# Optimization experiments

Hardware: AMD Instinct MI355X
Metric: run time of the kernel (lower is better)

Reference implementation:

```python
import jax, jax.numpy as jnp
import numpy as np

LOG_2PI = float(np.log(2.0 * np.pi))


def setup_inputs() -> dict:
    key = jax.random.key(0)
    k1, k2, k3 = jax.random.split(key, 3)
    N, D, K = 2_000_000, 16, 32
    data = jax.random.normal(k1, (N, D), dtype=jnp.float32)
    means = jax.random.uniform(k2, (K, D), dtype=jnp.float32)  # torch.rand init
    # torch init is eye expanded per component; perturb slightly so the
    # Cholesky / solve paths are exercised with non-trivial values while
    # A @ A.T stays well-conditioned PD.
    cov_parts = (jnp.eye(D, dtype=jnp.float32)[None, :, :]
                 + 0.1 * jax.random.normal(k3, (K, D, D), dtype=jnp.float32))
    log_weights = jnp.zeros((K,), dtype=jnp.float32)
    return {"data": data, "means": means, "cov_parts": cov_parts,
            "log_weights": log_weights}


def _mixture_loglik(data, means, cov_parts, log_weights):
    D = data.shape[-1]
    # covariance_k = A_k @ A_k^T  -> Cholesky factor L_k (lower)
    cov = jnp.einsum('kij,klj->kil', cov_parts, cov_parts)      # [K, D, D]
    chol = jnp.linalg.cholesky(cov)                             # [K, D, D]

    def comp_logprob(mu, L):
        # MVN log_prob for one component over all N points
        diff = data - mu                                        # [N, D]
        # solve L z = diff^T  -> z: [D, N]
        z = jax.scipy.linalg.solve_triangular(L, diff.T, lower=True)
        quad = jnp.sum(z * z, axis=0)                           # [N]
        logdet = jnp.sum(jnp.log(jnp.diagonal(L)))              # 0.5*logdet(cov)
        return -0.5 * (quad + D * LOG_2PI) - logdet             # [N]

    # [N, K] log-likelihood per point per component
    log_liks = jax.vmap(comp_logprob, in_axes=(0, 0), out_axes=1)(means, chol)
    weighted = log_liks + log_weights ** 2                      # note: squared, per source
    return jnp.mean(jax.nn.logsumexp(weighted, axis=1))


def reference(data, means, cov_parts, log_weights):
    return _mixture_loglik(data, means, cov_parts, log_weights)
```

## Files before the change

### kernel.cpp

```cpp
#include <hip/hip_runtime.h>
#include <math.h>


#define LOG_2PI 1.8378770664093453f
#define INV_LN2 1.4426950408889634f
#define LN2_D   0.6931471805599453

typedef float    float4v __attribute__((ext_vector_type(4)));
typedef float    f32x16  __attribute__((ext_vector_type(16)));
typedef _Float16 f16x8   __attribute__((ext_vector_type(8)));
typedef _Float16 f16x2   __attribute__((ext_vector_type(2)));

union H8 { f16x8 h8; f16x2 h2[4]; };

#if __has_builtin(__builtin_amdgcn_exp2f)
#define EXP2F(x) __builtin_amdgcn_exp2f(x)
#else
#define EXP2F(x) exp2f(x)
#endif
#if __has_builtin(__builtin_amdgcn_logf)
#define LOG2F(x) __builtin_amdgcn_logf(x)
#else
#define LOG2F(x) log2f(x)
#endif

static __device__ __forceinline__ f16x2 pk2(float a, float b) {
#if __has_builtin(__builtin_amdgcn_cvt_pkrtz)
  return __builtin_bit_cast(f16x2, __builtin_amdgcn_cvt_pkrtz(a, b));
#else
  f16x2 r; r[0] = (_Float16)a; r[1] = (_Float16)b; return r;
#endif
}

static __device__ __forceinline__ float partner32(float x, bool lo) {
#if __has_builtin(__builtin_amdgcn_permlane32_swap)
  typedef unsigned u32x2 __attribute__((ext_vector_type(2)));
  unsigned u = __builtin_bit_cast(unsigned, x);
  u32x2 r = __builtin_amdgcn_permlane32_swap(u, u, false, false);
  return __builtin_bit_cast(float, lo ? r[1] : r[0]);
#else
  return __shfl_xor(x, 32, 64);
#endif
}

static __device__ __forceinline__ f16x2 sel2(bool c, f16x2 a, f16x2 b) {
  unsigned ua = __builtin_bit_cast(unsigned, a);
  unsigned ub = __builtin_bit_cast(unsigned, b);
  return __builtin_bit_cast(f16x2, c ? ua : ub);
}

__global__ void setup_kernel(const float* __restrict__ means,
                             const float* __restrict__ cov_parts,
                             const float* __restrict__ log_weights,
                             _Float16* __restrict__ W)
{
  const int k = blockIdx.x;
  const int i = threadIdx.x;

  __shared__ float sA[16][17];
  __shared__ float sC[16][17];
  __shared__ float sMu[16];
  __shared__ float sR[16];

  if (i < 16) {
    #pragma unroll
    for (int j = 0; j < 16; ++j) sA[i][j] = cov_parts[(k*16 + i)*16 + j];
    sMu[i] = means[k*16 + i];
  }
  __syncthreads();

  if (i < 16) {
    #pragma unroll
    for (int j = 0; j < 16; ++j) {
      float acc = 0.f;
      #pragma unroll
      for (int l = 0; l < 16; ++l) acc += sA[i][l] * sA[j][l];
      sC[i][j] = acc;
    }
  }
  __syncthreads();

  for (int j = 0; j < 16; ++j) {
    if (i == j) {
      float d = sC[j][j];
      for (int l = 0; l < j; ++l) d -= sC[j][l]*sC[j][l];
      sC[j][j] = sqrtf(d);
    }
    __syncthreads();
    if (i < 16 && i > j) {
      float a = sC[i][j];
      for (int l = 0; l < j; ++l) a -= sC[i][l]*sC[j][l];
      sC[i][j] = a / sC[j][j];
    }
    __syncthreads();
  }

  if (i < 16) {
    float y[16];
    #pragma unroll
    for (int r = 0; r < 16; ++r) {
      float a = (r == i) ? 1.f : 0.f;
      #pragma unroll
      for (int l = 0; l < r; ++l) a -= sC[r][l] * y[l];
      y[r] = a / sC[r][r];
    }
    #pragma unroll
    for (int r = 0; r < 16; ++r) sA[r][i] = y[r];
  }
  __syncthreads();

  if (i < 16) {
    float p[16];
    #pragma unroll
    for (int j = 0; j < 16; ++j) {
      float acc = 0.f;
      #pragma unroll
      for (int l = 0; l < 16; ++l) acc += sA[l][i] * sA[l][j];
      p[j] = acc;
    }
    float ri = 0.f;
    #pragma unroll
    for (int j = 0; j < 16; ++j) ri += p[j] * sMu[j];
    sR[i] = ri;

    #pragma unroll
    for (int j = 0; j < 16; ++j) {
      W[(size_t)(i*64 + (k + 32*(j >> 3)))*8 + (j & 7)] =
          (_Float16)(-0.5f * INV_LN2 * p[j]);
    }
    W[(size_t)(16*64 + (k + 32*(i >> 3)))*8 + (i & 7)] =
        (_Float16)(INV_LN2 * ri);
  }
  __syncthreads();

  if (i == 0) {
    float logdet = 0.f;
    #pragma unroll
    for (int j = 0; j < 16; ++j) logdet += __logf(sC[j][j]);
    float mupmu = 0.f;
    #pragma unroll
    for (int j = 0; j < 16; ++j) mupmu += sMu[j] * sR[j];
    float lw = log_weights[k];
    float c2v = INV_LN2 * (-0.5f*(mupmu + 16.f*LOG_2PI) - logdet + lw*lw);
    #pragma unroll
    for (int v = 0; v < 8; ++v) {
      W[(size_t)(17*64 + k)*8 + v]      = (v == 0) ? (_Float16)c2v : (_Float16)0.f;
      W[(size_t)(17*64 + k + 32)*8 + v] = (_Float16)0.f;
    }
  }
}

__global__ __launch_bounds__(256, 2) void main_kernel(
    const float* __restrict__ data,
    const _Float16* __restrict__ W,
    float* __restrict__ partials,
    int npairs)
{
  const int lane = threadIdx.x & 63;
  const int n32  = lane & 31;
  const bool lo  = lane < 32;
  const int gwave  = (int)((blockIdx.x * blockDim.x + threadIdx.x) >> 6);
  const int nwaves = (int)((gridDim.x * blockDim.x) >> 6);

  f16x8 Wf[18];
  #pragma unroll
  for (int c = 0; c < 18; ++c)
    Wf[c] = *(const f16x8*)(W + (size_t)(c*64 + lane)*8);

  H8 bC;
  #pragma unroll
  for (int j = 0; j < 4; ++j) bC.h2[j] = pk2(0.f, 0.f);
  if (lo) bC.h2[0] = pk2(1.f, 0.f);

  float accsum = 0.f;

  const char* ptr = (const char*)data + ((size_t)gwave*4096 + (size_t)n32*64);
  const size_t step = (size_t)nwaves * 4096;

  float4v pA0, pA1, pA2, pA3, pB0, pB1, pB2, pB3;
  if (gwave < npairs) {
    pA0 = *(const float4v*)(ptr);        pA1 = *(const float4v*)(ptr + 16);
    pA2 = *(const float4v*)(ptr + 32);   pA3 = *(const float4v*)(ptr + 48);
    pB0 = *(const float4v*)(ptr + 2048); pB1 = *(const float4v*)(ptr + 2064);
    pB2 = *(const float4v*)(ptr + 2080); pB3 = *(const float4v*)(ptr + 2096);
  }

  for (int p = gwave; p < npairs; p += nwaves) {
    f16x2 xhA[8], xhB[8];
    xhA[0] = pk2(pA0[0], pA0[1]); xhA[1] = pk2(pA0[2], pA0[3]);
    xhA[2] = pk2(pA1[0], pA1[1]); xhA[3] = pk2(pA1[2], pA1[3]);
    xhA[4] = pk2(pA2[0], pA2[1]); xhA[5] = pk2(pA2[2], pA2[3]);
    xhA[6] = pk2(pA3[0], pA3[1]); xhA[7] = pk2(pA3[2], pA3[3]);
    xhB[0] = pk2(pB0[0], pB0[1]); xhB[1] = pk2(pB0[2], pB0[3]);
    xhB[2] = pk2(pB1[0], pB1[1]); xhB[3] = pk2(pB1[2], pB1[3]);
    xhB[4] = pk2(pB2[0], pB2[1]); xhB[5] = pk2(pB2[2], pB2[3]);
    xhB[6] = pk2(pB3[0], pB3[1]); xhB[7] = pk2(pB3[2], pB3[3]);

    ptr += step;
    if (p + nwaves < npairs) {
      pA0 = *(const float4v*)(ptr);        pA1 = *(const float4v*)(ptr + 16);
      pA2 = *(const float4v*)(ptr + 32);   pA3 = *(const float4v*)(ptr + 48);
      pB0 = *(const float4v*)(ptr + 2048); pB1 = *(const float4v*)(ptr + 2064);
      pB2 = *(const float4v*)(ptr + 2080); pB3 = *(const float4v*)(ptr + 2096);
    }

    f16x2 xsA[4], xsB[4];
    #pragma unroll
    for (int j = 0; j < 4; ++j) {
      xsA[j] = sel2(lo, xhA[j], xhA[4+j]);
      xsB[j] = sel2(lo, xhB[j], xhB[4+j]);
    }

    f32x16 accA, accB;
    #pragma unroll
    for (int r = 0; r < 16; ++r) { accA[r] = 0.f; accB[r] = 0.f; }

    #pragma unroll
    for (int c = 0; c < 16; ++c) {
      _Float16 xiA = xhA[c >> 1][c & 1];
      H8 bA;
      #pragma unroll
      for (int j = 0; j < 4; ++j) bA.h2[j] = xsA[j] * xiA;
      accA = __builtin_amdgcn_mfma_f32_32x32x16_f16(Wf[c], bA.h8, accA, 0, 0, 0);
      _Float16 xiB = xhB[c >> 1][c & 1];
      H8 bB;
      #pragma unroll
      for (int j = 0; j < 4; ++j) bB.h2[j] = xsB[j] * xiB;
      accB = __builtin_amdgcn_mfma_f32_32x32x16_f16(Wf[c], bB.h8, accB, 0, 0, 0);
    }
    {
      H8 bA, bB;
      #pragma unroll
      for (int j = 0; j < 4; ++j) { bA.h2[j] = xsA[j]; bB.h2[j] = xsB[j]; }
      accA = __builtin_amdgcn_mfma_f32_32x32x16_f16(Wf[16], bA.h8, accA, 0, 0, 0);
      accB = __builtin_amdgcn_mfma_f32_32x32x16_f16(Wf[16], bB.h8, accB, 0, 0, 0);
    }
    {
      accA = __builtin_amdgcn_mfma_f32_32x32x16_f16(Wf[17], bC.h8, accA, 0, 0, 0);
      accB = __builtin_amdgcn_mfma_f32_32x32x16_f16(Wf[17], bC.h8, accB, 0, 0, 0);
    }

    {
      float m = accA[0];
      #pragma unroll
      for (int r = 1; r < 16; ++r) m = fmaxf(m, accA[r]);
      m = fmaxf(m, partner32(m, lo));
      float s = 0.f;
      #pragma unroll
      for (int r = 0; r < 16; ++r) s += EXP2F(accA[r] - m);
      s += partner32(s, lo);
      accsum += m + LOG2F(s);
    }
    {
      float m = accB[0];
      #pragma unroll
      for (int r = 1; r < 16; ++r) m = fmaxf(m, accB[r]);
      m = fmaxf(m, partner32(m, lo));
      float s = 0.f;
      #pragma unroll
      for (int r = 0; r < 16; ++r) s += EXP2F(accB[r] - m);
      s += partner32(s, lo);
      accsum += m + LOG2F(s);
    }
  }

  #pragma unroll
  for (int off = 1; off <= 32; off <<= 1)
    accsum += __shfl_xor(accsum, off, 64);

  __shared__ float wsum[4];
  const int wid = (int)(threadIdx.x >> 6);
  if ((threadIdx.x & 63) == 0) wsum[wid] = accsum;
  __syncthreads();
  if (threadIdx.x == 0)
    partials[blockIdx.x] = wsum[0] + wsum[1] + wsum[2] + wsum[3];
}

__global__ void reduce_kernel(const float* __restrict__ partials, int n,
                              float* __restrict__ out, double scale)
{
  __shared__ double sd[256];
  double a = 0.0;
  for (int idx = threadIdx.x; idx < n; idx += 256) a += (double)partials[idx];
  sd[threadIdx.x] = a;
  __syncthreads();
  for (int s = 128; s > 0; s >>= 1) {
    if ((int)threadIdx.x < s) sd[threadIdx.x] += sd[threadIdx.x + s];
    __syncthreads();
  }
  if (threadIdx.x == 0) out[0] = (float)(sd[0] * scale);
}

extern "C" void kernel_launch(void* const* d_in, const int* in_sizes, int n_in,
                              void* d_out, int out_size, void* d_ws, size_t ws_size,
                              hipStream_t stream)
{
  const float* data        = (const float*)d_in[0];
  const float* means       = (const float*)d_in[1];
  const float* cov_parts   = (const float*)d_in[2];
  const float* log_weights = (const float*)d_in[3];

  const int npts   = in_sizes[0] / 16;
  const int npairs = npts / 64;

  _Float16* W      = (_Float16*)d_ws;
  float*    partials = (float*)((char*)d_ws + (size_t)18*64*8*sizeof(_Float16));

  const int GRID = 512, BLOCK = 256;
  setup_kernel<<<32, 64, 0, stream>>>(means, cov_parts, log_weights, W);
  main_kernel<<<GRID, BLOCK, 0, stream>>>(data, W, partials, npairs);
  reduce_kernel<<<1, 256, 0, stream>>>(partials, GRID, (float*)d_out,
                                       LN2_D / (2.0 * (double)npts));
}
```

Measured before the change: 202.2 us.

## Process one 32-point tile per wave iteration and raise occupancy

Each wave iteration now handles a single 32-point tile instead of two interleaved 32-point tiles, which halves the accumulator and prefetch register state. Launch bounds go from 2 to 3 blocks per SIMD and the grid from 512 to 768 blocks, so more waves can hide memory latency. The cost is less instruction-level parallelism inside each wave, since two independent MFMA chains no longer overlap, and a smaller per-wave prefetch.

```diff
diff --git a/kernel.cpp b/kernel.cpp
--- a/kernel.cpp
+++ b/kernel.cpp
@@ -150,11 +150,11 @@
   }
 }
 
-__global__ __launch_bounds__(256, 2) void main_kernel(
+__global__ __launch_bounds__(256, 3) void main_kernel(
     const float* __restrict__ data,
     const _Float16* __restrict__ W,
     float* __restrict__ partials,
-    int npairs)
+    int ntiles)
 {
   const int lane = threadIdx.x & 63;
   const int n32  = lane & 31;
@@ -174,94 +174,61 @@
 
   float accsum = 0.f;
 
-  const char* ptr = (const char*)data + ((size_t)gwave*4096 + (size_t)n32*64);
-  const size_t step = (size_t)nwaves * 4096;
-
-  float4v pA0, pA1, pA2, pA3, pB0, pB1, pB2, pB3;
-  if (gwave < npairs) {
-    pA0 = *(const float4v*)(ptr);        pA1 = *(const float4v*)(ptr + 16);
-    pA2 = *(const float4v*)(ptr + 32);   pA3 = *(const float4v*)(ptr + 48);
-    pB0 = *(const float4v*)(ptr + 2048); pB1 = *(const float4v*)(ptr + 2064);
-    pB2 = *(const float4v*)(ptr + 2080); pB3 = *(const float4v*)(ptr + 2096);
-  }
-
-  for (int p = gwave; p < npairs; p += nwaves) {
-    f16x2 xhA[8], xhB[8];
-    xhA[0] = pk2(pA0[0], pA0[1]); xhA[1] = pk2(pA0[2], pA0[3]);
-    xhA[2] = pk2(pA1[0], pA1[1]); xhA[3] = pk2(pA1[2], pA1[3]);
-    xhA[4] = pk2(pA2[0], pA2[1]); xhA[5] = pk2(pA2[2], pA2[3]);
-    xhA[6] = pk2(pA3[0], pA3[1]); xhA[7] = pk2(pA3[2], pA3[3]);
-    xhB[0] = pk2(pB0[0], pB0[1]); xhB[1] = pk2(pB0[2], pB0[3]);
-    xhB[2] = pk2(pB1[0], pB1[1]); xhB[3] = pk2(pB1[2], pB1[3]);
-    xhB[4] = pk2(pB2[0], pB2[1]); xhB[5] = pk2(pB2[2], pB2[3]);
-    xhB[6] = pk2(pB3[0], pB3[1]); xhB[7] = pk2(pB3[2], pB3[3]);
+  const char* ptr = (const char*)data + ((size_t)gwave*2048 + (size_t)n32*64);
+  const size_t step = (size_t)nwaves * 2048;
+
+  float4v p0, p1, p2, p3;
+  if (gwave < ntiles) {
+    p0 = *(const float4v*)(ptr);      p1 = *(const float4v*)(ptr + 16);
+    p2 = *(const float4v*)(ptr + 32); p3 = *(const float4v*)(ptr + 48);
+  }
+
+  for (int t = gwave; t < ntiles; t += nwaves) {
+    f16x2 xh[8];
+    xh[0] = pk2(p0[0], p0[1]); xh[1] = pk2(p0[2], p0[3]);
+    xh[2] = pk2(p1[0], p1[1]); xh[3] = pk2(p1[2], p1[3]);
+    xh[4] = pk2(p2[0], p2[1]); xh[5] = pk2(p2[2], p2[3]);
+    xh[6] = pk2(p3[0], p3[1]); xh[7] = pk2(p3[2], p3[3]);
 
     ptr += step;
-    if (p + nwaves < npairs) {
-      pA0 = *(const float4v*)(ptr);        pA1 = *(const float4v*)(ptr + 16);
-      pA2 = *(const float4v*)(ptr + 32);   pA3 = *(const float4v*)(ptr + 48);
-      pB0 = *(const float4v*)(ptr + 2048); pB1 = *(const float4v*)(ptr + 2064);
-      pB2 = *(const float4v*)(ptr + 2080); pB3 = *(const float4v*)(ptr + 2096);
-    }
-
-    f16x2 xsA[4], xsB[4];
-    #pragma unroll
-    for (int j = 0; j < 4; ++j) {
-      xsA[j] = sel2(lo, xhA[j], xhA[4+j]);
-      xsB[j] = sel2(lo, xhB[j], xhB[4+j]);
-    }
-
-    f32x16 accA, accB;
-    #pragma unroll
-    for (int r = 0; r < 16; ++r) { accA[r] = 0.f; accB[r] = 0.f; }
+    if (t + nwaves < ntiles) {
+      p0 = *(const float4v*)(ptr);      p1 = *(const float4v*)(ptr + 16);
+      p2 = *(const float4v*)(ptr + 32); p3 = *(const float4v*)(ptr + 48);
+    }
+
+    f16x2 xs[4];
+    #pragma unroll
+    for (int j = 0; j < 4; ++j) xs[j] = sel2(lo, xh[j], xh[4+j]);
+
+    f32x16 acc;
+    #pragma unroll
+    for (int r = 0; r < 16; ++r) acc[r] = 0.f;
 
     #pragma unroll
     for (int c = 0; c < 16; ++c) {
-      _Float16 xiA = xhA[c >> 1][c & 1];
-      H8 bA;
-      #pragma unroll
-      for (int j = 0; j < 4; ++j) bA.h2[j] = xsA[j] * xiA;
-      accA = __builtin_amdgcn_mfma_f32_32x32x16_f16(Wf[c], bA.h8, accA, 0, 0, 0);
-      _Float16 xiB = xhB[c >> 1][c & 1];
-      H8 bB;
-      #pragma unroll
-      for (int j = 0; j < 4; ++j) bB.h2[j] = xsB[j] * xiB;
-      accB = __builtin_amdgcn_mfma_f32_32x32x16_f16(Wf[c], bB.h8, accB, 0, 0, 0);
+      _Float16 xi = xh[c >> 1][c & 1];
+      H8 b;
+      #pragma unroll
+      for (int j = 0; j < 4; ++j) b.h2[j] = xs[j] * xi;
+      acc = __builtin_amdgcn_mfma_f32_32x32x16_f16(Wf[c], b.h8, acc, 0, 0, 0);
     }
     {
-      H8 bA, bB;
-      #pragma unroll
-      for (int j = 0; j < 4; ++j) { bA.h2[j] = xsA[j]; bB.h2[j] = xsB[j]; }
-      accA = __builtin_amdgcn_mfma_f32_32x32x16_f16(Wf[16], bA.h8, accA, 0, 0, 0);
-      accB = __builtin_amdgcn_mfma_f32_32x32x16_f16(Wf[16], bB.h8, accB, 0, 0, 0);
-    }
-    {
-      accA = __builtin_amdgcn_mfma_f32_32x32x16_f16(Wf[17], bC.h8, accA, 0, 0, 0);
-      accB = __builtin_amdgcn_mfma_f32_32x32x16_f16(Wf[17], bC.h8, accB, 0, 0, 0);
-    }
-
-    {
-      float m = accA[0];
-      #pragma unroll
-      for (int r = 1; r < 16; ++r) m = fmaxf(m, accA[r]);
-      m = fmaxf(m, partner32(m, lo));
-      float s = 0.f;
-      #pragma unroll
-      for (int r = 0; r < 16; ++r) s += EXP2F(accA[r] - m);
-      s += partner32(s, lo);
-      accsum += m + LOG2F(s);
-    }
-    {
-      float m = accB[0];
-      #pragma unroll
-      for (int r = 1; r < 16; ++r) m = fmaxf(m, accB[r]);
-      m = fmaxf(m, partner32(m, lo));
-      float s = 0.f;
-      #pragma unroll
-      for (int r = 0; r < 16; ++r) s += EXP2F(accB[r] - m);
-      s += partner32(s, lo);
-      accsum += m + LOG2F(s);
-    }
+      H8 b;
+      #pragma unroll
+      for (int j = 0; j < 4; ++j) b.h2[j] = xs[j];
+      acc = __builtin_amdgcn_mfma_f32_32x32x16_f16(Wf[16], b.h8, acc, 0, 0, 0);
+    }
+    acc = __builtin_amdgcn_mfma_f32_32x32x16_f16(Wf[17], bC.h8, acc, 0, 0, 0);
+
+    float m = acc[0];
+    #pragma unroll
+    for (int r = 1; r < 16; ++r) m = fmaxf(m, acc[r]);
+    m = fmaxf(m, partner32(m, lo));
+    float s = 0.f;
+    #pragma unroll
+    for (int r = 0; r < 16; ++r) s += EXP2F(acc[r] - m);
+    s += partner32(s, lo);
+    accsum += m + LOG2F(s);
   }
 
   #pragma unroll
@@ -301,14 +268,14 @@
   const float* log_weights = (const float*)d_in[3];
 
   const int npts   = in_sizes[0] / 16;
-  const int npairs = npts / 64;
+  const int ntiles = npts / 32;
 
   _Float16* W      = (_Float16*)d_ws;
   float*    partials = (float*)((char*)d_ws + (size_t)18*64*8*sizeof(_Float16));
 
-  const int GRID = 512, BLOCK = 256;
+  const int GRID = 768, BLOCK = 256;
   setup_kernel<<<32, 64, 0, stream>>>(means, cov_parts, log_weights, W);
-  main_kernel<<<GRID, BLOCK, 0, stream>>>(data, W, partials, npairs);
+  main_kernel<<<GRID, BLOCK, 0, stream>>>(data, W, partials, ntiles);
   reduce_kernel<<<1, 256, 0, stream>>>(partials, GRID, (float*)d_out,
                                        LN2_D / (2.0 * (double)npts));
 }
```

Result: no change. 202.8 us (+0.3%).
